# Kernel tuning notes

Hardware: AMD Instinct MI355X
Metric: run time of the kernel (lower is better)

Reference implementation:

```python
import jax, jax.numpy as jnp
import numpy as np

NPOINT, K = 1024, 16
BN_EPS = 1e-5


def farthest_point_sample(xyz, npoint):
    # xyz: [B, N, 3]. Deterministic start at index 0 (torch version uses randint).
    B, N, _ = xyz.shape

    def step(carry, _):
        distance, farthest = carry
        centroid = jnp.take_along_axis(xyz, farthest[:, None, None], axis=1)  # [B,1,3]
        dist = jnp.sum((xyz - centroid) ** 2, axis=-1)  # [B,N]
        distance = jnp.minimum(distance, dist)
        nxt = jnp.argmax(distance, axis=-1)
        return (distance, nxt), farthest

    init = (jnp.full((B, N), 1e10, dtype=xyz.dtype), jnp.zeros((B,), dtype=jnp.int32))
    _, cents = jax.lax.scan(step, init, None, length=npoint)
    return jnp.transpose(cents)  # [B, npoint]


def knn_idx(k, xyz, new_xyz):
    # squared distances [B,S,N] via ||a||^2 + ||b||^2 - 2 a.b (avoids [B,S,N,3] blowup)
    d = (jnp.sum(new_xyz ** 2, -1)[:, :, None]
         + jnp.sum(xyz ** 2, -1)[:, None, :]
         - 2.0 * jnp.einsum('bsc,bnc->bsn', new_xyz, xyz))
    _, idx = jax.lax.top_k(-d, k)  # k smallest distances
    return idx


def gather_points(points, idx):
    # points: [B,N,C], idx: [B,...] -> [B,...,C]
    return jax.vmap(lambda p, i: p[i])(points, idx)


def bn_train(x, gamma, beta):
    # BatchNorm1d in train mode: batch statistics, biased variance
    m = jnp.mean(x, axis=0)
    v = jnp.var(x, axis=0)
    return gamma * (x - m) * jax.lax.rsqrt(v + BN_EPS) + beta


def setup_inputs() -> dict:
    key = jax.random.key(0)
    ks = jax.random.split(key, 16)
    B, N, CIN, COUT = 8, 4096, 64, 128
    cin3 = CIN + 3          # 67
    ec = int(cin3 * 2.0)    # 134 (expand_ratio=2, hidden_ch arg is unused by InvResMLP)
    s = 0.05
    return {
        'xyz': jax.random.normal(ks[0], (B, N, 3), jnp.float32),
        'pts': jax.random.normal(ks[1], (B, N, CIN), jnp.float32),
        'fc1_w': jax.random.normal(ks[2], (cin3, ec), jnp.float32) * s,
        'fc1_b': jnp.zeros((ec,), jnp.float32),
        'bn1_g': jnp.ones((ec,), jnp.float32),
        'bn1_b': jnp.zeros((ec,), jnp.float32),
        'fc2_w': jax.random.normal(ks[3], (ec, ec), jnp.float32) * s,
        'fc2_b': jnp.zeros((ec,), jnp.float32),
        'bn2_g': jnp.ones((ec,), jnp.float32),
        'bn2_b': jnp.zeros((ec,), jnp.float32),
        'fc3_w': jax.random.normal(ks[4], (ec, COUT), jnp.float32) * s,
        'fc3_b': jnp.zeros((COUT,), jnp.float32),
        'bn3_g': jnp.ones((COUT,), jnp.float32),
        'bn3_b': jnp.zeros((COUT,), jnp.float32),
        'sc_w': jax.random.normal(ks[5], (cin3, COUT), jnp.float32) * s,
        'sc_b': jnp.zeros((COUT,), jnp.float32),
        'scbn_g': jnp.ones((COUT,), jnp.float32),
        'scbn_b': jnp.zeros((COUT,), jnp.float32),
    }


def reference(xyz, pts, fc1_w, fc1_b, bn1_g, bn1_b, fc2_w, fc2_b, bn2_g, bn2_b,
              fc3_w, fc3_b, bn3_g, bn3_b, sc_w, sc_b, scbn_g, scbn_b):
    # --- local_group: FPS + kNN grouping ---
    cent = farthest_point_sample(xyz, NPOINT)          # [B,S]
    new_xyz = gather_points(xyz, cent)                 # [B,S,3]
    idx = knn_idx(K, xyz, new_xyz)                     # [B,S,K]
    grouped_xyz = gather_points(xyz, idx)              # [B,S,K,3]
    grouped_pts = gather_points(pts, idx)              # [B,S,K,C]
    grouped_xyz_norm = grouped_xyz - new_xyz[:, :, None, :]
    x = jnp.concatenate([grouped_xyz_norm, grouped_pts], axis=-1)  # [B,S,K,C+3]

    # --- InvResMLP (pointwise, train-mode BN, dropout as identity) ---
    B, S, Kk, C = x.shape
    x = x.reshape(B * S * Kk, C)
    sc = bn_train(x @ sc_w + sc_b, scbn_g, scbn_b)
    h = jax.nn.relu(bn_train(x @ fc1_w + fc1_b, bn1_g, bn1_b))
    h = jax.nn.relu(bn_train(h @ fc2_w + fc2_b, bn2_g, bn2_b))
    h = bn_train(h @ fc3_w + fc3_b, bn3_g, bn3_b)
    h = jax.nn.relu(h + sc)
    feats = h.reshape(B, S, Kk, -1)

    new_pts = jnp.max(feats, axis=2)                   # [B,S,out_ch]
    return new_xyz, new_pts
```

## Files before the change

kernel.cpp:

```cpp
#include <hip/hip_runtime.h>
#include <cstdint>
#include <cstddef>

typedef short short8 __attribute__((ext_vector_type(8)));
typedef float f32x4 __attribute__((ext_vector_type(4)));
typedef unsigned long long u64x2 __attribute__((ext_vector_type(2)));

#define B_   8
#define N_   4096
#define S_   1024
#define K_   16
#define M_   131072
#define CIN_ 64

__device__ inline float bf2f(unsigned short u) {
    unsigned int v = ((unsigned int)u) << 16;
    return __builtin_bit_cast(float, v);
}
__device__ inline unsigned short f2bf(float f) {
    unsigned int u = __builtin_bit_cast(unsigned int, f);
    unsigned int lsb = (u >> 16) & 1u;
    u += 0x7fffu + lsb;
    return (unsigned short)(u >> 16);
}

template<int CTRL>
__device__ inline float dpp_maxf(float x) {
    int xi = __builtin_bit_cast(int, x);
    int yi = __builtin_amdgcn_update_dpp(0, xi, CTRL, 0xF, 0xF, true);
    return fmaxf(x, __builtin_bit_cast(float, yi));
}

__global__ __launch_bounds__(256) void fps_aux_kernel(
    const float* __restrict__ xyz, float* __restrict__ outxyz,
    const float* __restrict__ fc1_w, const float* __restrict__ sc_w,
    const float* __restrict__ fc2_w, const float* __restrict__ fc3_w,
    unsigned short* __restrict__ WT1, unsigned short* __restrict__ WT2,
    unsigned short* __restrict__ WT3, float* __restrict__ sqn)
{
    __shared__ float px_s[N_], py_s[N_], pz_s[N_];
    __shared__ float sOut[S_ * 3];
    __shared__ __attribute__((aligned(16))) unsigned long long sK[2][4];
    int t = threadIdx.x;

    if (blockIdx.x >= 8) {
        int aux = blockIdx.x - 8;
#pragma unroll
        for (int ch = 0; ch < 10; ch++) {
            int idx = (aux * 10 + ch) * 256 + t;
            if (idx < 13824) {
                int row = idx / 96, k = idx % 96;
                WT1[idx] = f2bf((k < 67 && row < 134) ? fc1_w[k * 134 + row] : 0.0f);
            } else if (idx < 26112) {
                int j = idx - 13824;
                int row = j / 96, k = j % 96;
                WT1[13824 + j] = f2bf((k < 67) ? sc_w[k * 128 + row] : 0.0f);
            } else if (idx < 49152) {
                int j = idx - 26112;
                int row = j / 160, k = j % 160;
                WT2[j] = f2bf((k < 134 && row < 134) ? fc2_w[k * 134 + row] : 0.0f);
            } else if (idx < 69632) {
                int j = idx - 49152;
                int row = j / 160, k = j % 160;
                WT3[j] = f2bf((k < 134) ? fc3_w[k * 128 + row] : 0.0f);
            } else {
                int i = idx - 69632;
                float x = xyz[i * 3 + 0], y = xyz[i * 3 + 1], z = xyz[i * 3 + 2];
                sqn[i] = __fadd_rn(__fadd_rn(__fmul_rn(x, x), __fmul_rn(y, y)),
                                   __fmul_rn(z, z));
            }
        }
        return;
    }

    int b = blockIdx.x;
    const float* xb = xyz + (size_t)b * N_ * 3;
    int w = t >> 6, l = t & 63;
    const int NP = 16;
    float px[NP], py[NP], pz[NP], dst[NP];
    {
        float flat[48];
        const float4* xb4 = (const float4*)xb + t * 12;
#pragma unroll
        for (int j = 0; j < 12; j++) {
            float4 v = xb4[j];
            flat[j * 4 + 0] = v.x; flat[j * 4 + 1] = v.y;
            flat[j * 4 + 2] = v.z; flat[j * 4 + 3] = v.w;
        }
#pragma unroll
        for (int i = 0; i < NP; i++) {
            int p = t * 16 + i;
            px[i] = flat[i * 3 + 0];
            py[i] = flat[i * 3 + 1];
            pz[i] = flat[i * 3 + 2];
            dst[i] = 1e10f;
            px_s[p] = px[i]; py_s[p] = py[i]; pz_s[p] = pz[i];
            asm volatile("" : "+v"(px[i]), "+v"(py[i]), "+v"(pz[i]));
        }
    }
    __syncthreads();
    float cx = px_s[0], cy = py_s[0], cz = pz_s[0];
    for (int s = 0; s < S_; s++) {
        if (t == 0) { sOut[s * 3 + 0] = cx; sOut[s * 3 + 1] = cy; sOut[s * 3 + 2] = cz; }
        if (s == S_ - 1) break;
        float bd = -1.0f; int bi = 0;
#pragma unroll
        for (int i = 0; i < NP; i++) {
            float dx = __fsub_rn(px[i], cx);
            float dy = __fsub_rn(py[i], cy);
            float dz = __fsub_rn(pz[i], cz);
            float d  = __fadd_rn(__fadd_rn(__fmul_rn(dx, dx), __fmul_rn(dy, dy)),
                                 __fmul_rn(dz, dz));
            float nd = fminf(dst[i], d);
            dst[i] = nd;
            if (nd > bd) bi = i;
            bd = fmaxf(bd, nd);
        }
        float m = bd;
        m = dpp_maxf<0xB1>(m);
        m = dpp_maxf<0x4E>(m);
        m = dpp_maxf<0x141>(m);
        m = dpp_maxf<0x140>(m);
        m = dpp_maxf<0x142>(m);
        m = dpp_maxf<0x143>(m);
        float bw = __builtin_bit_cast(float,
                       __builtin_amdgcn_readlane(__builtin_bit_cast(int, m), 63));
        unsigned long long msk = __ballot(bd == bw);
        int wl  = (int)__builtin_ctzll(msk);
        int wbi = __builtin_amdgcn_readlane(bi, wl);
        int pw  = (w * 64 + wl) * 16 + wbi;
        unsigned long long key =
            ((unsigned long long)__builtin_bit_cast(unsigned, bw) << 32) |
            (unsigned long long)(unsigned)(4095 - pw);
        int par = s & 1;
        if (l == 0) sK[par][w] = key;
        __syncthreads();
        u64x2 kA = *(u64x2*)&sK[par][0];
        u64x2 kB = *(u64x2*)&sK[par][2];
        unsigned long long ka = kA[0] > kA[1] ? kA[0] : kA[1];
        unsigned long long kb = kB[0] > kB[1] ? kB[0] : kB[1];
        unsigned long long g  = ka > kb ? ka : kb;
        int p = 4095 - (int)(g & 0xFFFu);
        cx = px_s[p]; cy = py_s[p]; cz = pz_s[p];
    }
    __syncthreads();
    float* ob = outxyz + (size_t)b * S_ * 3;
    for (int i = t; i < S_ * 3; i += 256) ob[i] = sOut[i];
}

__global__ __launch_bounds__(256) void knn_build(const float* __restrict__ xyz,
                                                 const float* __restrict__ sqn,
                                                 const float* __restrict__ newxyz,
                                                 const float* __restrict__ pts,
                                                 unsigned short* __restrict__ X)
{
    __shared__ int sNbr[4][16];
    int w = threadIdx.x >> 6, l = threadIdx.x & 63;
    int q = blockIdx.x * 4 + w;
    int b = q >> 10;
    const float* xb = xyz + (size_t)b * N_ * 3;
    const float* sb = sqn + (size_t)b * N_;
    float qx = newxyz[(size_t)q * 3 + 0];
    float qy = newxyz[(size_t)q * 3 + 1];
    float qz = newxyz[(size_t)q * 3 + 2];
    float sa = __fadd_rn(__fadd_rn(__fmul_rn(qx, qx), __fmul_rn(qy, qy)), __fmul_rn(qz, qz));

    float d16[16]; int i16[16];
#pragma unroll
    for (int j = 0; j < 16; j++) { d16[j] = 3.0e38f; i16[j] = -1; }
    for (int i = 0; i < N_ / 64; i++) {
        int n = i * 64 + l;
        float bx = xb[n * 3 + 0], by = xb[n * 3 + 1], bz = xb[n * 3 + 2];
        float dot = __fmaf_rn(qz, bz, __fmaf_rn(qy, by, __fmul_rn(qx, bx)));
        float d = __fsub_rn(__fadd_rn(sa, sb[n]), __fmul_rn(2.0f, dot));
        if (d < d16[0]) {
            d16[0] = d; i16[0] = n;
#pragma unroll
            for (int j = 0; j < 15; j++) {
                if (d16[j] < d16[j + 1]) {
                    float td = d16[j]; d16[j] = d16[j + 1]; d16[j + 1] = td;
                    int   ti = i16[j]; i16[j] = i16[j + 1]; i16[j + 1] = ti;
                }
            }
        }
    }
#pragma unroll
    for (int r = 0; r < 16; r++) {
        float cd = d16[15]; int cn = i16[15];
#pragma unroll
        for (int off = 1; off < 64; off <<= 1) {
            float od = __shfl_xor(cd, off);
            int   on = __shfl_xor(cn, off);
            if (od < cd || (od == cd && on < cn)) { cd = od; cn = on; }
        }
        if (l == 0) sNbr[w][r] = cn;
        if (i16[15] == cn) {
#pragma unroll
            for (int j = 15; j >= 1; j--) { d16[j] = d16[j - 1]; i16[j] = i16[j - 1]; }
            d16[0] = 3.0e38f; i16[0] = -1;
        }
    }
    __syncthreads();
    int row = l >> 2, seg = l & 3;
    int n = sNbr[w][row];
    const float* pr = pts + ((size_t)b * N_ + n) * CIN_;
    const float* xr = xyz + ((size_t)b * N_ + n) * 3;
    float v[24];
#pragma unroll
    for (int e = 0; e < 24; e++) {
        int c = seg * 24 + e;
        float val;
        if (c == 0)      val = xr[0] - qx;
        else if (c == 1) val = xr[1] - qy;
        else if (c == 2) val = xr[2] - qz;
        else if (c < 67) val = pr[c - 3];
        else             val = 0.0f;
        v[e] = val;
    }
    short8 s0, s1, s2;
#pragma unroll
    for (int e = 0; e < 8; e++) {
        s0[e] = (short)f2bf(v[e]);
        s1[e] = (short)f2bf(v[8 + e]);
        s2[e] = (short)f2bf(v[16 + e]);
    }
    unsigned short* xp = X + ((size_t)q * 16 + row) * 96 + seg * 24;
    *(short8*)xp = s0;
    *(short8*)(xp + 8) = s1;
    *(short8*)(xp + 16) = s2;
}

template<int KPAD, int NF, bool BNST>
__device__ __forceinline__ void gemm_core(
    const unsigned short* __restrict__ A, const unsigned short* __restrict__ Wt,
    unsigned short* __restrict__ Zo, float* __restrict__ sum, float* __restrict__ sq,
    int nreal, const float* __restrict__ ps, const float* __restrict__ pq,
    const float* __restrict__ pg, const float* __restrict__ pb,
    int r0, unsigned short* sBuf, float* sSt, float* sAC, int t)
{
    constexpr int AST = KPAD + 8;
    for (int i = t; i < NF * 32; i += 256) sSt[i] = 0.0f;
    if (BNST) {
        if (t < 160) {
            float a = 0.f, c = 0.f;
            if (t < 134) {
                const float inv = 1.0f / (float)M_;
                float m = ps[t] * inv;
                float var = pq[t] * inv - m * m;
                a = pg[t] * rsqrtf(var + 1e-5f);
                c = pb[t] - a * m;
            }
            sAC[2 * t] = a; sAC[2 * t + 1] = c;
        }
        __syncthreads();
#pragma unroll
        for (int c8 = 0; c8 < 10; c8++) {
            int chunk = c8 * 256 + t;
            int row = chunk / 20, col0 = (chunk % 20) * 8;
            short8 hv = {0, 0, 0, 0, 0, 0, 0, 0};
            if (col0 < 144) {
                short8 zv = *(const short8*)(A + (size_t)(r0 + row) * 144 + col0);
#pragma unroll
                for (int e = 0; e < 8; e++) {
                    float2 ac = *(float2*)&sAC[2 * (col0 + e)];
                    float v = fmaxf(ac.x * bf2f((unsigned short)zv[e]) + ac.y, 0.0f);
                    hv[e] = (short)f2bf(v);
                }
            }
            *(short8*)(sBuf + row * AST + col0) = hv;
        }
    } else {
#pragma unroll
        for (int c8 = 0; c8 < (128 * KPAD / 8) / 256; c8++) {
            int chunk = c8 * 256 + t;
            int row = chunk / (KPAD / 8), col0 = (chunk % (KPAD / 8)) * 8;
            *(short8*)(sBuf + row * AST + col0) =
                *(const short8*)(A + (size_t)(r0 + row) * KPAD + col0);
        }
    }
    __syncthreads();
    int w = t >> 6, l = t & 63, lhi = l >> 4, llo = l & 15;
    f32x4 acc[2][NF];
#pragma unroll
    for (int m = 0; m < 2; m++)
#pragma unroll
        for (int n = 0; n < NF; n++) acc[m][n] = (f32x4){0.f, 0.f, 0.f, 0.f};
#pragma unroll
    for (int ks = 0; ks < KPAD / 32; ks++) {
        short8 bfr[NF];
#pragma unroll
        for (int n = 0; n < NF; n++)
            bfr[n] = *(const short8*)(Wt + (size_t)(n * 16 + llo) * KPAD + ks * 32 + lhi * 8);
#pragma unroll
        for (int m = 0; m < 2; m++) {
            short8 afr = *(const short8*)(sBuf + (w * 32 + m * 16 + llo) * AST + ks * 32 + lhi * 8);
#pragma unroll
            for (int n = 0; n < NF; n++)
                acc[m][n] = __builtin_amdgcn_mfma_f32_16x16x32_bf16(afr, bfr[n], acc[m][n], 0, 0, 0);
        }
    }
    __syncthreads();
    constexpr int OST = NF * 16 + 8;
#pragma unroll
    for (int n = 0; n < NF; n++) {
        int c = n * 16 + llo;
        float ss = 0.f, sqv = 0.f;
#pragma unroll
        for (int m = 0; m < 2; m++) {
#pragma unroll
            for (int j = 0; j < 4; j++) {
                float v = acc[m][n][j];
                int row = w * 32 + m * 16 + lhi * 4 + j;
                sBuf[row * OST + c] = f2bf(v);
                ss += v; sqv += v * v;
            }
        }
        ss += __shfl_xor(ss, 16); ss += __shfl_xor(ss, 32);
        sqv += __shfl_xor(sqv, 16); sqv += __shfl_xor(sqv, 32);
        if (l < 16) { atomicAdd(&sSt[c * 2], ss); atomicAdd(&sSt[c * 2 + 1], sqv); }
    }
    __syncthreads();
#pragma unroll
    for (int c8 = 0; c8 < NF; c8++) {
        int chunk = c8 * 256 + t;
        int row = chunk / (NF * 2), cc = chunk % (NF * 2);
        *(short8*)(Zo + (size_t)(r0 + row) * (NF * 16) + cc * 8) =
            *(const short8*)(sBuf + row * OST + cc * 8);
    }
    for (int c = t; c < NF * 16; c += 256) {
        if (c < nreal) {
            atomicAdd(&sum[c], sSt[c * 2]);
            atomicAdd(&sq[c], sSt[c * 2 + 1]);
        }
    }
}

__global__ __launch_bounds__(256) void gemm1_fused(
    const unsigned short* __restrict__ X, const unsigned short* __restrict__ WT1,
    unsigned short* __restrict__ Z1, unsigned short* __restrict__ ZSC,
    float* s1, float* q1, float* ssc, float* qsc)
{
    __shared__ unsigned short sBuf[21504];
    __shared__ float sSt[288];
    int t = threadIdx.x;
    if (blockIdx.x < 1024)
        gemm_core<96, 9, false>(X, WT1, Z1, s1, q1, 134,
                                nullptr, nullptr, nullptr, nullptr,
                                blockIdx.x * 128, sBuf, sSt, nullptr, t);
    else
        gemm_core<96, 8, false>(X, WT1 + 13824, ZSC, ssc, qsc, 128,
                                nullptr, nullptr, nullptr, nullptr,
                                (blockIdx.x - 1024) * 128, sBuf, sSt, nullptr, t);
}

__global__ __launch_bounds__(256) void gemm_l2(
    const unsigned short* __restrict__ Zin, const unsigned short* __restrict__ WT,
    unsigned short* __restrict__ Zout, float* sum, float* sq,
    const float* ps, const float* pq, const float* pg, const float* pb)
{
    __shared__ unsigned short sBuf[21504];
    __shared__ float sSt[288];
    __shared__ float sAC[320];
    gemm_core<160, 9, true>(Zin, WT, Zout, sum, sq, 134, ps, pq, pg, pb,
                            blockIdx.x * 128, sBuf, sSt, sAC, threadIdx.x);
}

__global__ __launch_bounds__(256) void gemm_l3(
    const unsigned short* __restrict__ Zin, const unsigned short* __restrict__ WT,
    unsigned short* __restrict__ Zout, float* sum, float* sq,
    const float* ps, const float* pq, const float* pg, const float* pb)
{
    __shared__ unsigned short sBuf[21504];
    __shared__ float sSt[288];
    __shared__ float sAC[320];
    gemm_core<160, 8, true>(Zin, WT, Zout, sum, sq, 128, ps, pq, pg, pb,
                            blockIdx.x * 128, sBuf, sSt, sAC, threadIdx.x);
}

__global__ __launch_bounds__(256) void final_kernel(
    const unsigned short* __restrict__ Z3, const unsigned short* __restrict__ ZSC,
    const float* __restrict__ sum3, const float* __restrict__ sq3,
    const float* __restrict__ g3, const float* __restrict__ b3,
    const float* __restrict__ sumsc, const float* __restrict__ sqsc,
    const float* __restrict__ gsc, const float* __restrict__ bsc,
    float* __restrict__ out)
{
    __shared__ float sF[512];
    int t = threadIdx.x;
    if (t < 128) {
        const float inv = 1.0f / (float)M_;
        float m3 = sum3[t] * inv, v3 = sq3[t] * inv - m3 * m3;
        float a3 = g3[t] * rsqrtf(v3 + 1e-5f), c3 = b3[t] - a3 * m3;
        float ms = sumsc[t] * inv, vs = sqsc[t] * inv - ms * ms;
        float as = gsc[t] * rsqrtf(vs + 1e-5f), cs = bsc[t] - as * ms;
        sF[t * 4 + 0] = a3; sF[t * 4 + 1] = c3; sF[t * 4 + 2] = as; sF[t * 4 + 3] = cs;
    }
    __syncthreads();
    int tid = blockIdx.x * 256 + t;
    int bs = tid >> 4, ch0 = (tid & 15) * 8;
    float A3[8], C3[8], AS[8], CS[8], mx[8];
#pragma unroll
    for (int e = 0; e < 8; e++) {
        f32x4 f = *(f32x4*)&sF[(ch0 + e) * 4];
        A3[e] = f[0]; C3[e] = f[1]; AS[e] = f[2]; CS[e] = f[3];
        mx[e] = 0.0f;
    }
    const unsigned short* z3p = Z3 + (size_t)bs * 16 * 128 + ch0;
    const unsigned short* zsp = ZSC + (size_t)bs * 16 * 128 + ch0;
#pragma unroll
    for (int k = 0; k < 16; k++) {
        short8 z3 = *(const short8*)(z3p + (size_t)k * 128);
        short8 zs = *(const short8*)(zsp + (size_t)k * 128);
#pragma unroll
        for (int e = 0; e < 8; e++) {
            float y = fmaxf(A3[e] * bf2f((unsigned short)z3[e]) + C3[e]
                            + AS[e] * bf2f((unsigned short)zs[e]) + CS[e], 0.0f);
            mx[e] = fmaxf(mx[e], y);
        }
    }
    float* op = out + 24576 + (size_t)bs * 128 + ch0;
#pragma unroll
    for (int e = 0; e < 8; e++) op[e] = mx[e];
}

#define WS_STATS 0
#define WS_WT1   8192
#define WS_WT2   61440
#define WS_WT3   108544
#define WS_SQN   149760
#define WS_X     281088
#define WS_Z1    25447424
#define WS_ZSC   63196416
#define WS_Z2    96751104

extern "C" void kernel_launch(void* const* d_in, const int* in_sizes, int n_in,
                              void* d_out, int out_size, void* d_ws, size_t ws_size,
                              hipStream_t stream)
{
    const float* xyz    = (const float*)d_in[0];
    const float* pts    = (const float*)d_in[1];
    const float* fc1_w  = (const float*)d_in[2];
    const float* bn1_g  = (const float*)d_in[4];
    const float* bn1_b  = (const float*)d_in[5];
    const float* fc2_w  = (const float*)d_in[6];
    const float* bn2_g  = (const float*)d_in[8];
    const float* bn2_b  = (const float*)d_in[9];
    const float* fc3_w  = (const float*)d_in[10];
    const float* bn3_g  = (const float*)d_in[12];
    const float* bn3_b  = (const float*)d_in[13];
    const float* sc_w   = (const float*)d_in[14];
    const float* scbn_g = (const float*)d_in[16];
    const float* scbn_b = (const float*)d_in[17];

    char* ws = (char*)d_ws;
    float* st = (float*)(ws + WS_STATS);
    float* bn1_sum = st + 0,    *bn1_sq = st + 136;
    float* bnsc_sum = st + 272, *bnsc_sq = st + 400;
    float* bn2_sum = st + 528,  *bn2_sq = st + 664;
    float* bn3_sum = st + 800,  *bn3_sq = st + 928;

    unsigned short* WT1 = (unsigned short*)(ws + WS_WT1);
    unsigned short* WT2 = (unsigned short*)(ws + WS_WT2);
    unsigned short* WT3 = (unsigned short*)(ws + WS_WT3);
    float* SQN = (float*)(ws + WS_SQN);
    unsigned short* X   = (unsigned short*)(ws + WS_X);
    unsigned short* Z1  = (unsigned short*)(ws + WS_Z1);
    unsigned short* ZSC = (unsigned short*)(ws + WS_ZSC);
    unsigned short* Z2  = (unsigned short*)(ws + WS_Z2);
    unsigned short* Z3  = Z1;
    float* out = (float*)d_out;

    hipMemsetAsync(ws + WS_STATS, 0, 1056 * 4, stream);

    fps_aux_kernel<<<48, 256, 0, stream>>>(xyz, out, fc1_w, sc_w, fc2_w, fc3_w,
                                           WT1, WT2, WT3, SQN);
    knn_build<<<2048, 256, 0, stream>>>(xyz, SQN, out, pts, X);

    gemm1_fused<<<2048, 256, 0, stream>>>(X, WT1, Z1, ZSC,
                                          bn1_sum, bn1_sq, bnsc_sum, bnsc_sq);
    gemm_l2<<<1024, 256, 0, stream>>>(Z1, WT2, Z2, bn2_sum, bn2_sq,
                                      bn1_sum, bn1_sq, bn1_g, bn1_b);
    gemm_l3<<<1024, 256, 0, stream>>>(Z2, WT3, Z3, bn3_sum, bn3_sq,
                                      bn2_sum, bn2_sq, bn2_g, bn2_b);

    final_kernel<<<512, 256, 0, stream>>>(Z3, ZSC, bn3_sum, bn3_sq, bn3_g, bn3_b,
                                          bnsc_sum, bnsc_sq, scbn_g, scbn_b, out);
}
```

Before: 958.0 us.

## Fuse pipeline into cooperative persistent megakernel overlapping FPS with kNN

Replaces the six-kernel sequence with a single cooperative persistent kernel. Eight blocks run farthest-point sampling and publish progress watermarks every 64 centroids. Worker blocks spin on those watermarks so kNN grouping runs alongside FPS, and the GEMM and BN layers are separated by software grid barriers. The change targets the serial FPS latency and the launch gaps between stages. It adds spin-wait and grid-barrier overhead, limits the grid to 512 blocks, and keeps the old launch path as a fallback if the cooperative launch fails. It also swaps the bf16 packing to v_cvt_pk_bf16_f32.

```diff
diff --git a/kernel.cpp b/kernel.cpp
--- a/kernel.cpp
+++ b/kernel.cpp
@@ -23,12 +23,435 @@
     u += 0x7fffu + lsb;
     return (unsigned short)(u >> 16);
 }
+__device__ inline unsigned cvtpk_bf16(float lo, float hi) {
+    unsigned r; asm("v_cvt_pk_bf16_f32 %0, %1, %2" : "=v"(r) : "v"(lo), "v"(hi)); return r;
+}
+__device__ inline short8 pack8_bf16(const float* v) {
+    uint4 u;
+    u.x = cvtpk_bf16(v[0], v[1]); u.y = cvtpk_bf16(v[2], v[3]);
+    u.z = cvtpk_bf16(v[4], v[5]); u.w = cvtpk_bf16(v[6], v[7]);
+    return __builtin_bit_cast(short8, u);
+}
 
 template<int CTRL>
 __device__ inline float dpp_maxf(float x) {
     int xi = __builtin_bit_cast(int, x);
     int yi = __builtin_amdgcn_update_dpp(0, xi, CTRL, 0xF, 0xF, true);
     return fmaxf(x, __builtin_bit_cast(float, yi));
+}
+
+template<int KPAD, int NF, bool BNST>
+__device__ __forceinline__ void gemm_core(
+    const unsigned short* __restrict__ A, const unsigned short* __restrict__ Wt,
+    unsigned short* __restrict__ Zo, float* __restrict__ sum, float* __restrict__ sq,
+    int nreal, const float* __restrict__ ps, const float* __restrict__ pq,
+    const float* __restrict__ pg, const float* __restrict__ pb,
+    int r0, unsigned short* sBuf, float* sSt, float* sAC, int t)
+{
+    __syncthreads();
+    constexpr int AST = KPAD + 8;
+    for (int i = t; i < NF * 32; i += 256) sSt[i] = 0.0f;
+    if (BNST) {
+        if (t < 160) {
+            float a = 0.f, c = 0.f;
+            if (t < 134) {
+                const float inv = 1.0f / (float)M_;
+                float m = ps[t] * inv;
+                float var = pq[t] * inv - m * m;
+                a = pg[t] * rsqrtf(var + 1e-5f);
+                c = pb[t] - a * m;
+            }
+            sAC[2 * t] = a; sAC[2 * t + 1] = c;
+        }
+        __syncthreads();
+#pragma unroll
+        for (int c8 = 0; c8 < 10; c8++) {
+            int chunk = c8 * 256 + t;
+            int row = chunk / 20, col0 = (chunk % 20) * 8;
+            short8 hv = {0, 0, 0, 0, 0, 0, 0, 0};
+            if (col0 < 144) {
+                short8 zv = *(const short8*)(A + (size_t)(r0 + row) * 144 + col0);
+                float tmp[8];
+#pragma unroll
+                for (int e = 0; e < 8; e++) {
+                    float2 ac = *(float2*)&sAC[2 * (col0 + e)];
+                    tmp[e] = fmaxf(ac.x * bf2f((unsigned short)zv[e]) + ac.y, 0.0f);
+                }
+                hv = pack8_bf16(tmp);
+            }
+            *(short8*)(sBuf + row * AST + col0) = hv;
+        }
+    } else {
+#pragma unroll
+        for (int c8 = 0; c8 < (128 * KPAD / 8) / 256; c8++) {
+            int chunk = c8 * 256 + t;
+            int row = chunk / (KPAD / 8), col0 = (chunk % (KPAD / 8)) * 8;
+            *(short8*)(sBuf + row * AST + col0) =
+                *(const short8*)(A + (size_t)(r0 + row) * KPAD + col0);
+        }
+    }
+    __syncthreads();
+    int w = t >> 6, l = t & 63, lhi = l >> 4, llo = l & 15;
+    f32x4 acc[2][NF];
+#pragma unroll
+    for (int m = 0; m < 2; m++)
+#pragma unroll
+        for (int n = 0; n < NF; n++) acc[m][n] = (f32x4){0.f, 0.f, 0.f, 0.f};
+#pragma unroll
+    for (int ks = 0; ks < KPAD / 32; ks++) {
+        short8 bfr[NF];
+#pragma unroll
+        for (int n = 0; n < NF; n++)
+            bfr[n] = *(const short8*)(Wt + (size_t)(n * 16 + llo) * KPAD + ks * 32 + lhi * 8);
+#pragma unroll
+        for (int m = 0; m < 2; m++) {
+            short8 afr = *(const short8*)(sBuf + (w * 32 + m * 16 + llo) * AST + ks * 32 + lhi * 8);
+#pragma unroll
+            for (int n = 0; n < NF; n++)
+                acc[m][n] = __builtin_amdgcn_mfma_f32_16x16x32_bf16(afr, bfr[n], acc[m][n], 0, 0, 0);
+        }
+    }
+    __syncthreads();
+    constexpr int OST = NF * 16 + 8;
+#pragma unroll
+    for (int n = 0; n < NF; n++) {
+        int c = n * 16 + llo;
+        float ss = 0.f, sqv = 0.f;
+#pragma unroll
+        for (int m = 0; m < 2; m++) {
+#pragma unroll
+            for (int j = 0; j < 4; j++) {
+                float v = acc[m][n][j];
+                int row = w * 32 + m * 16 + lhi * 4 + j;
+                sBuf[row * OST + c] = f2bf(v);
+                ss += v; sqv += v * v;
+            }
+        }
+        ss += __shfl_xor(ss, 16); ss += __shfl_xor(ss, 32);
+        sqv += __shfl_xor(sqv, 16); sqv += __shfl_xor(sqv, 32);
+        if (l < 16) { atomicAdd(&sSt[c * 2], ss); atomicAdd(&sSt[c * 2 + 1], sqv); }
+    }
+    __syncthreads();
+#pragma unroll
+    for (int c8 = 0; c8 < NF; c8++) {
+        int chunk = c8 * 256 + t;
+        int row = chunk / (NF * 2), cc = chunk % (NF * 2);
+        *(short8*)(Zo + (size_t)(r0 + row) * (NF * 16) + cc * 8) =
+            *(const short8*)(sBuf + row * OST + cc * 8);
+    }
+    for (int c = t; c < NF * 16; c += 256) {
+        if (c < nreal) {
+            atomicAdd(&sum[c], sSt[c * 2]);
+            atomicAdd(&sq[c], sSt[c * 2 + 1]);
+        }
+    }
+}
+
+__device__ inline void gridbar(int* cnt, int* gen, int nblk, int t)
+{
+    __syncthreads();
+    __threadfence();
+    if (t == 0) {
+        int g = __hip_atomic_load(gen, __ATOMIC_RELAXED, __HIP_MEMORY_SCOPE_AGENT);
+        if (__hip_atomic_fetch_add(cnt, 1, __ATOMIC_ACQ_REL, __HIP_MEMORY_SCOPE_AGENT) == nblk - 1) {
+            __hip_atomic_store(cnt, 0, __ATOMIC_RELAXED, __HIP_MEMORY_SCOPE_AGENT);
+            __hip_atomic_store(gen, g + 1, __ATOMIC_RELEASE, __HIP_MEMORY_SCOPE_AGENT);
+        } else {
+            while (__hip_atomic_load(gen, __ATOMIC_ACQUIRE, __HIP_MEMORY_SCOPE_AGENT) == g)
+                __builtin_amdgcn_s_sleep(8);
+        }
+    }
+    __syncthreads();
+    __threadfence();
+}
+
+struct MegaArgs {
+    const float *xyz, *pts, *fc1_w, *sc_w, *fc2_w, *fc3_w;
+    const float *bn1_g, *bn1_b, *bn2_g, *bn2_b, *bn3_g, *bn3_b, *scbn_g, *scbn_b;
+    unsigned short *WT1, *WT2, *WT3;
+    float *SQN;
+    unsigned short *X, *Z1, *ZSC, *Z2;
+    float *st; int *wm; int *bar_cnt; int *bar_gen;
+    float *out;
+    int workers;
+};
+
+__global__ __launch_bounds__(256) void mega(MegaArgs A)
+{
+    __shared__ __attribute__((aligned(16))) char smem[61952];
+    int t = threadIdx.x;
+    int bid = blockIdx.x;
+    int nblk = gridDim.x;
+
+    float* st = A.st;
+    float* bn1_sum = st + 0,    *bn1_sq = st + 136;
+    float* bnsc_sum = st + 272, *bnsc_sq = st + 400;
+    float* bn2_sum = st + 528,  *bn2_sq = st + 664;
+    float* bn3_sum = st + 800,  *bn3_sq = st + 928;
+
+    if (bid < 8) {
+        float* px_s = (float*)smem;
+        float* py_s = px_s + 4096;
+        float* pz_s = px_s + 8192;
+        float* sOut = (float*)(smem + 49152);
+        unsigned long long* sK = (unsigned long long*)(smem + 61440);
+        int b = bid;
+        const float* xb = A.xyz + (size_t)b * N_ * 3;
+        float* ob = A.out + (size_t)b * S_ * 3;
+        int w = t >> 6, l = t & 63;
+        float px[16], py[16], pz[16], dst[16];
+        {
+            float flat[48];
+            const float4* xb4 = (const float4*)xb + t * 12;
+#pragma unroll
+            for (int j = 0; j < 12; j++) {
+                float4 v = xb4[j];
+                flat[j * 4 + 0] = v.x; flat[j * 4 + 1] = v.y;
+                flat[j * 4 + 2] = v.z; flat[j * 4 + 3] = v.w;
+            }
+#pragma unroll
+            for (int i = 0; i < 16; i++) {
+                int p = t * 16 + i;
+                px[i] = flat[i * 3 + 0];
+                py[i] = flat[i * 3 + 1];
+                pz[i] = flat[i * 3 + 2];
+                dst[i] = 1e10f;
+                px_s[p] = px[i]; py_s[p] = py[i]; pz_s[p] = pz[i];
+                asm volatile("" : "+v"(px[i]), "+v"(py[i]), "+v"(pz[i]));
+            }
+        }
+        __syncthreads();
+        float cx = px_s[0], cy = py_s[0], cz = pz_s[0];
+        for (int s = 0; s < S_; s++) {
+            if (t == 0) { sOut[s * 3 + 0] = cx; sOut[s * 3 + 1] = cy; sOut[s * 3 + 2] = cz; }
+            if ((s & 63) == 63 && w == 0) {
+                int base = (s - 63) * 3;
+                if (l < 48) {
+                    float4 v = *(float4*)&sOut[base + l * 4];
+                    *(float4*)&ob[base + l * 4] = v;
+                }
+                __threadfence();
+                if (t == 0)
+                    __hip_atomic_store(A.wm + b * 16, s + 1, __ATOMIC_RELEASE,
+                                       __HIP_MEMORY_SCOPE_AGENT);
+            }
+            if (s == S_ - 1) break;
+            float bd = -1.0f; int bi = 0;
+#pragma unroll
+            for (int i = 0; i < 16; i++) {
+                float dx = __fsub_rn(px[i], cx);
+                float dy = __fsub_rn(py[i], cy);
+                float dz = __fsub_rn(pz[i], cz);
+                float d  = __fadd_rn(__fadd_rn(__fmul_rn(dx, dx), __fmul_rn(dy, dy)),
+                                     __fmul_rn(dz, dz));
+                float nd = fminf(dst[i], d);
+                dst[i] = nd;
+                if (nd > bd) bi = i;
+                bd = fmaxf(bd, nd);
+            }
+            float m = bd;
+            m = dpp_maxf<0xB1>(m);
+            m = dpp_maxf<0x4E>(m);
+            m = dpp_maxf<0x141>(m);
+            m = dpp_maxf<0x140>(m);
+            m = dpp_maxf<0x142>(m);
+            m = dpp_maxf<0x143>(m);
+            float bw = __builtin_bit_cast(float,
+                           __builtin_amdgcn_readlane(__builtin_bit_cast(int, m), 63));
+            unsigned long long msk = __ballot(bd == bw);
+            int wl  = (int)__builtin_ctzll(msk);
+            int wbi = __builtin_amdgcn_readlane(bi, wl);
+            int pw  = (w * 64 + wl) * 16 + wbi;
+            unsigned long long key =
+                ((unsigned long long)__builtin_bit_cast(unsigned, bw) << 32) |
+                (unsigned long long)(unsigned)(4095 - pw);
+            int par = s & 1;
+            if (l == 0) sK[par * 4 + w] = key;
+            __syncthreads();
+            u64x2 kA = *(u64x2*)&sK[par * 4 + 0];
+            u64x2 kB = *(u64x2*)&sK[par * 4 + 2];
+            unsigned long long ka = kA[0] > kA[1] ? kA[0] : kA[1];
+            unsigned long long kb = kB[0] > kB[1] ? kB[0] : kB[1];
+            unsigned long long g  = ka > kb ? ka : kb;
+            int p = 4095 - (int)(g & 0xFFFu);
+            cx = px_s[p]; cy = py_s[p]; cz = pz_s[p];
+        }
+    } else {
+        int wk = bid - 8;
+        if (wk < 40) {
+#pragma unroll
+            for (int ch = 0; ch < 10; ch++) {
+                int idx = (wk * 10 + ch) * 256 + t;
+                if (idx < 13824) {
+                    int row = idx / 96, k = idx % 96;
+                    A.WT1[idx] = f2bf((k < 67 && row < 134) ? A.fc1_w[k * 134 + row] : 0.0f);
+                } else if (idx < 26112) {
+                    int j = idx - 13824;
+                    int row = j / 96, k = j % 96;
+                    A.WT1[13824 + j] = f2bf((k < 67) ? A.sc_w[k * 128 + row] : 0.0f);
+                } else if (idx < 49152) {
+                    int j = idx - 26112;
+                    int row = j / 160, k = j % 160;
+                    A.WT2[j] = f2bf((k < 134 && row < 134) ? A.fc2_w[k * 134 + row] : 0.0f);
+                } else if (idx < 69632) {
+                    int j = idx - 49152;
+                    int row = j / 160, k = j % 160;
+                    A.WT3[j] = f2bf((k < 134) ? A.fc3_w[k * 128 + row] : 0.0f);
+                }
+            }
+        }
+        float* sqnL = (float*)smem;
+        int* sNbr = (int*)(smem + 16384);
+        int b = wk & 7;
+        const float* xb = A.xyz + (size_t)b * N_ * 3;
+#pragma unroll
+        for (int i = 0; i < 16; i++) {
+            int p = i * 256 + t;
+            float x = xb[p * 3 + 0], y = xb[p * 3 + 1], z = xb[p * 3 + 2];
+            sqnL[p] = __fadd_rn(__fadd_rn(__fmul_rn(x, x), __fmul_rn(y, y)),
+                                __fmul_rn(z, z));
+        }
+        __syncthreads();
+        int w = t >> 6, l = t & 63;
+        for (int G = wk; G < 2048; G += A.workers) {
+            int sidx = (G >> 3) * 4 + w;
+            int q = b * 1024 + sidx;
+            while (__hip_atomic_load(A.wm + b * 16, __ATOMIC_ACQUIRE,
+                                     __HIP_MEMORY_SCOPE_AGENT) <= sidx)
+                __builtin_amdgcn_s_sleep(32);
+            float qx = A.out[(size_t)q * 3 + 0];
+            float qy = A.out[(size_t)q * 3 + 1];
+            float qz = A.out[(size_t)q * 3 + 2];
+            float sa = __fadd_rn(__fadd_rn(__fmul_rn(qx, qx), __fmul_rn(qy, qy)),
+                                 __fmul_rn(qz, qz));
+            float d16[16]; int i16[16];
+#pragma unroll
+            for (int j = 0; j < 16; j++) { d16[j] = 3.0e38f; i16[j] = -1; }
+            for (int i = 0; i < N_ / 64; i++) {
+                int n = i * 64 + l;
+                float bx = xb[n * 3 + 0], by = xb[n * 3 + 1], bz = xb[n * 3 + 2];
+                float dot = __fmaf_rn(qz, bz, __fmaf_rn(qy, by, __fmul_rn(qx, bx)));
+                float d = __fsub_rn(__fadd_rn(sa, sqnL[n]), __fmul_rn(2.0f, dot));
+                if (d < d16[0]) {
+                    d16[0] = d; i16[0] = n;
+#pragma unroll
+                    for (int j = 0; j < 15; j++) {
+                        if (d16[j] < d16[j + 1]) {
+                            float td = d16[j]; d16[j] = d16[j + 1]; d16[j + 1] = td;
+                            int   ti = i16[j]; i16[j] = i16[j + 1]; i16[j + 1] = ti;
+                        }
+                    }
+                }
+            }
+#pragma unroll
+            for (int r = 0; r < 16; r++) {
+                float cd = d16[15]; int cn = i16[15];
+#pragma unroll
+                for (int off = 1; off < 64; off <<= 1) {
+                    float od = __shfl_xor(cd, off);
+                    int   on = __shfl_xor(cn, off);
+                    if (od < cd || (od == cd && on < cn)) { cd = od; cn = on; }
+                }
+                if (l == 0) sNbr[w * 16 + r] = cn;
+                if (i16[15] == cn) {
+#pragma unroll
+                    for (int j = 15; j >= 1; j--) { d16[j] = d16[j - 1]; i16[j] = i16[j - 1]; }
+                    d16[0] = 3.0e38f; i16[0] = -1;
+                }
+            }
+            __syncthreads();
+            int row = l >> 2, seg = l & 3;
+            int n = sNbr[w * 16 + row];
+            const float* pr = A.pts + ((size_t)b * N_ + n) * CIN_;
+            const float* xr = A.xyz + ((size_t)b * N_ + n) * 3;
+            float v[24];
+#pragma unroll
+            for (int e = 0; e < 24; e++) {
+                int c = seg * 24 + e;
+                float val;
+                if (c == 0)      val = xr[0] - qx;
+                else if (c == 1) val = xr[1] - qy;
+                else if (c == 2) val = xr[2] - qz;
+                else if (c < 67) val = pr[c - 3];
+                else             val = 0.0f;
+                v[e] = val;
+            }
+            short8 s0 = pack8_bf16(v), s1 = pack8_bf16(v + 8), s2 = pack8_bf16(v + 16);
+            unsigned short* xp = A.X + ((size_t)q * 16 + row) * 96 + seg * 24;
+            *(short8*)xp = s0;
+            *(short8*)(xp + 8) = s1;
+            *(short8*)(xp + 16) = s2;
+            __syncthreads();
+        }
+    }
+    gridbar(A.bar_cnt, A.bar_gen, nblk, t);
+
+    {
+        unsigned short* sBuf = (unsigned short*)smem;
+        float* sSt = (float*)(smem + 43008);
+        float* sAC = (float*)(smem + 44160);
+        for (int tile = bid; tile < 2048; tile += nblk) {
+            if (tile < 1024)
+                gemm_core<96, 9, false>(A.X, A.WT1, A.Z1, bn1_sum, bn1_sq, 134,
+                                        nullptr, nullptr, nullptr, nullptr,
+                                        tile * 128, sBuf, sSt, sAC, t);
+            else
+                gemm_core<96, 8, false>(A.X, A.WT1 + 13824, A.ZSC, bnsc_sum, bnsc_sq, 128,
+                                        nullptr, nullptr, nullptr, nullptr,
+                                        (tile - 1024) * 128, sBuf, sSt, sAC, t);
+        }
+        gridbar(A.bar_cnt, A.bar_gen, nblk, t);
+        for (int tile = bid; tile < 1024; tile += nblk)
+            gemm_core<160, 9, true>(A.Z1, A.WT2, A.Z2, bn2_sum, bn2_sq, 134,
+                                    bn1_sum, bn1_sq, A.bn1_g, A.bn1_b,
+                                    tile * 128, sBuf, sSt, sAC, t);
+        gridbar(A.bar_cnt, A.bar_gen, nblk, t);
+        for (int tile = bid; tile < 1024; tile += nblk)
+            gemm_core<160, 8, true>(A.Z2, A.WT3, A.Z1 , bn3_sum, bn3_sq, 128,
+                                    bn2_sum, bn2_sq, A.bn2_g, A.bn2_b,
+                                    tile * 128, sBuf, sSt, sAC, t);
+        gridbar(A.bar_cnt, A.bar_gen, nblk, t);
+    }
+
+    {
+        float* sF = (float*)smem;
+        if (t < 128) {
+            const float inv = 1.0f / (float)M_;
+            float m3 = bn3_sum[t] * inv, v3 = bn3_sq[t] * inv - m3 * m3;
+            float a3 = A.bn3_g[t] * rsqrtf(v3 + 1e-5f), c3 = A.bn3_b[t] - a3 * m3;
+            float ms = bnsc_sum[t] * inv, vs = bnsc_sq[t] * inv - ms * ms;
+            float as = A.scbn_g[t] * rsqrtf(vs + 1e-5f), cs = A.scbn_b[t] - as * ms;
+            sF[t * 4 + 0] = a3; sF[t * 4 + 1] = c3; sF[t * 4 + 2] = as; sF[t * 4 + 3] = cs;
+        }
+        __syncthreads();
+        for (int c = bid; c < 512; c += nblk) {
+            int tid = c * 256 + t;
+            int bs = tid >> 4, ch0 = (tid & 15) * 8;
+            float A3[8], C3[8], AS[8], CS[8], mx[8];
+#pragma unroll
+            for (int e = 0; e < 8; e++) {
+                f32x4 f = *(f32x4*)&sF[(ch0 + e) * 4];
+                A3[e] = f[0]; C3[e] = f[1]; AS[e] = f[2]; CS[e] = f[3];
+                mx[e] = 0.0f;
+            }
+            const unsigned short* z3p = A.Z1 + (size_t)bs * 16 * 128 + ch0;
+            const unsigned short* zsp = A.ZSC + (size_t)bs * 16 * 128 + ch0;
+#pragma unroll
+            for (int k = 0; k < 16; k++) {
+                short8 z3 = *(const short8*)(z3p + (size_t)k * 128);
+                short8 zs = *(const short8*)(zsp + (size_t)k * 128);
+#pragma unroll
+                for (int e = 0; e < 8; e++) {
+                    float y = fmaxf(A3[e] * bf2f((unsigned short)z3[e]) + C3[e]
+                                    + AS[e] * bf2f((unsigned short)zs[e]) + CS[e], 0.0f);
+                    mx[e] = fmaxf(mx[e], y);
+                }
+            }
+            float* op = A.out + 24576 + (size_t)bs * 128 + ch0;
+#pragma unroll
+            for (int e = 0; e < 8; e++) op[e] = mx[e];
+        }
+    }
 }
 
 __global__ __launch_bounds__(256) void fps_aux_kernel(
@@ -42,7 +465,6 @@
     __shared__ float sOut[S_ * 3];
     __shared__ __attribute__((aligned(16))) unsigned long long sK[2][4];
     int t = threadIdx.x;
-
     if (blockIdx.x >= 8) {
         int aux = blockIdx.x - 8;
 #pragma unroll
@@ -72,12 +494,10 @@
         }
         return;
     }
-
     int b = blockIdx.x;
     const float* xb = xyz + (size_t)b * N_ * 3;
     int w = t >> 6, l = t & 63;
-    const int NP = 16;
-    float px[NP], py[NP], pz[NP], dst[NP];
+    float px[16], py[16], pz[16], dst[16];
     {
         float flat[48];
         const float4* xb4 = (const float4*)xb + t * 12;
@@ -88,11 +508,9 @@
             flat[j * 4 + 2] = v.z; flat[j * 4 + 3] = v.w;
         }
 #pragma unroll
-        for (int i = 0; i < NP; i++) {
+        for (int i = 0; i < 16; i++) {
             int p = t * 16 + i;
-            px[i] = flat[i * 3 + 0];
-            py[i] = flat[i * 3 + 1];
-            pz[i] = flat[i * 3 + 2];
+            px[i] = flat[i * 3 + 0]; py[i] = flat[i * 3 + 1]; pz[i] = flat[i * 3 + 2];
             dst[i] = 1e10f;
             px_s[p] = px[i]; py_s[p] = py[i]; pz_s[p] = pz[i];
             asm volatile("" : "+v"(px[i]), "+v"(py[i]), "+v"(pz[i]));
@@ -105,7 +523,7 @@
         if (s == S_ - 1) break;
         float bd = -1.0f; int bi = 0;
 #pragma unroll
-        for (int i = 0; i < NP; i++) {
+        for (int i = 0; i < 16; i++) {
             float dx = __fsub_rn(px[i], cx);
             float dy = __fsub_rn(py[i], cy);
             float dz = __fsub_rn(pz[i], cz);
@@ -117,12 +535,8 @@
             bd = fmaxf(bd, nd);
         }
         float m = bd;
-        m = dpp_maxf<0xB1>(m);
-        m = dpp_maxf<0x4E>(m);
-        m = dpp_maxf<0x141>(m);
-        m = dpp_maxf<0x140>(m);
-        m = dpp_maxf<0x142>(m);
-        m = dpp_maxf<0x143>(m);
+        m = dpp_maxf<0xB1>(m); m = dpp_maxf<0x4E>(m); m = dpp_maxf<0x141>(m);
+        m = dpp_maxf<0x140>(m); m = dpp_maxf<0x142>(m); m = dpp_maxf<0x143>(m);
         float bw = __builtin_bit_cast(float,
                        __builtin_amdgcn_readlane(__builtin_bit_cast(int, m), 63));
         unsigned long long msk = __ballot(bd == bw);
@@ -164,7 +578,6 @@
     float qy = newxyz[(size_t)q * 3 + 1];
     float qz = newxyz[(size_t)q * 3 + 2];
     float sa = __fadd_rn(__fadd_rn(__fmul_rn(qx, qx), __fmul_rn(qy, qy)), __fmul_rn(qz, qz));
-
     float d16[16]; int i16[16];
 #pragma unroll
     for (int j = 0; j < 16; j++) { d16[j] = 3.0e38f; i16[j] = -1; }
@@ -217,124 +630,13 @@
         else             val = 0.0f;
         v[e] = val;
     }
-    short8 s0, s1, s2;
-#pragma unroll
-    for (int e = 0; e < 8; e++) {
-        s0[e] = (short)f2bf(v[e]);
-        s1[e] = (short)f2bf(v[8 + e]);
-        s2[e] = (short)f2bf(v[16 + e]);
-    }
+    short8 s0 = pack8_bf16(v), s1 = pack8_bf16(v + 8), s2 = pack8_bf16(v + 16);
     unsigned short* xp = X + ((size_t)q * 16 + row) * 96 + seg * 24;
     *(short8*)xp = s0;
     *(short8*)(xp + 8) = s1;
     *(short8*)(xp + 16) = s2;
 }
 
-template<int KPAD, int NF, bool BNST>
-__device__ __forceinline__ void gemm_core(
-    const unsigned short* __restrict__ A, const unsigned short* __restrict__ Wt,
-    unsigned short* __restrict__ Zo, float* __restrict__ sum, float* __restrict__ sq,
-    int nreal, const float* __restrict__ ps, const float* __restrict__ pq,
-    const float* __restrict__ pg, const float* __restrict__ pb,
-    int r0, unsigned short* sBuf, float* sSt, float* sAC, int t)
-{
-    constexpr int AST = KPAD + 8;
-    for (int i = t; i < NF * 32; i += 256) sSt[i] = 0.0f;
-    if (BNST) {
-        if (t < 160) {
-            float a = 0.f, c = 0.f;
-            if (t < 134) {
-                const float inv = 1.0f / (float)M_;
-                float m = ps[t] * inv;
-                float var = pq[t] * inv - m * m;
-                a = pg[t] * rsqrtf(var + 1e-5f);
-                c = pb[t] - a * m;
-            }
-            sAC[2 * t] = a; sAC[2 * t + 1] = c;
-        }
-        __syncthreads();
-#pragma unroll
-        for (int c8 = 0; c8 < 10; c8++) {
-            int chunk = c8 * 256 + t;
-            int row = chunk / 20, col0 = (chunk % 20) * 8;
-            short8 hv = {0, 0, 0, 0, 0, 0, 0, 0};
-            if (col0 < 144) {
-                short8 zv = *(const short8*)(A + (size_t)(r0 + row) * 144 + col0);
-#pragma unroll
-                for (int e = 0; e < 8; e++) {
-                    float2 ac = *(float2*)&sAC[2 * (col0 + e)];
-                    float v = fmaxf(ac.x * bf2f((unsigned short)zv[e]) + ac.y, 0.0f);
-                    hv[e] = (short)f2bf(v);
-                }
-            }
-            *(short8*)(sBuf + row * AST + col0) = hv;
-        }
-    } else {
-#pragma unroll
-        for (int c8 = 0; c8 < (128 * KPAD / 8) / 256; c8++) {
-            int chunk = c8 * 256 + t;
-            int row = chunk / (KPAD / 8), col0 = (chunk % (KPAD / 8)) * 8;
-            *(short8*)(sBuf + row * AST + col0) =
-                *(const short8*)(A + (size_t)(r0 + row) * KPAD + col0);
-        }
-    }
-    __syncthreads();
-    int w = t >> 6, l = t & 63, lhi = l >> 4, llo = l & 15;
-    f32x4 acc[2][NF];
-#pragma unroll
-    for (int m = 0; m < 2; m++)
-#pragma unroll
-        for (int n = 0; n < NF; n++) acc[m][n] = (f32x4){0.f, 0.f, 0.f, 0.f};
-#pragma unroll
-    for (int ks = 0; ks < KPAD / 32; ks++) {
-        short8 bfr[NF];
-#pragma unroll
-        for (int n = 0; n < NF; n++)
-            bfr[n] = *(const short8*)(Wt + (size_t)(n * 16 + llo) * KPAD + ks * 32 + lhi * 8);
-#pragma unroll
-        for (int m = 0; m < 2; m++) {
-            short8 afr = *(const short8*)(sBuf + (w * 32 + m * 16 + llo) * AST + ks * 32 + lhi * 8);
-#pragma unroll
-            for (int n = 0; n < NF; n++)
-                acc[m][n] = __builtin_amdgcn_mfma_f32_16x16x32_bf16(afr, bfr[n], acc[m][n], 0, 0, 0);
-        }
-    }
-    __syncthreads();
-    constexpr int OST = NF * 16 + 8;
-#pragma unroll
-    for (int n = 0; n < NF; n++) {
-        int c = n * 16 + llo;
-        float ss = 0.f, sqv = 0.f;
-#pragma unroll
-        for (int m = 0; m < 2; m++) {
-#pragma unroll
-            for (int j = 0; j < 4; j++) {
-                float v = acc[m][n][j];
-                int row = w * 32 + m * 16 + lhi * 4 + j;
-                sBuf[row * OST + c] = f2bf(v);
-                ss += v; sqv += v * v;
-            }
-        }
-        ss += __shfl_xor(ss, 16); ss += __shfl_xor(ss, 32);
-        sqv += __shfl_xor(sqv, 16); sqv += __shfl_xor(sqv, 32);
-        if (l < 16) { atomicAdd(&sSt[c * 2], ss); atomicAdd(&sSt[c * 2 + 1], sqv); }
-    }
-    __syncthreads();
-#pragma unroll
-    for (int c8 = 0; c8 < NF; c8++) {
-        int chunk = c8 * 256 + t;
-        int row = chunk / (NF * 2), cc = chunk % (NF * 2);
-        *(short8*)(Zo + (size_t)(r0 + row) * (NF * 16) + cc * 8) =
-            *(const short8*)(sBuf + row * OST + cc * 8);
-    }
-    for (int c = t; c < NF * 16; c += 256) {
-        if (c < nreal) {
-            atomicAdd(&sum[c], sSt[c * 2]);
-            atomicAdd(&sq[c], sSt[c * 2 + 1]);
-        }
-    }
-}
-
 __global__ __launch_bounds__(256) void gemm1_fused(
     const unsigned short* __restrict__ X, const unsigned short* __restrict__ WT1,
     unsigned short* __restrict__ Z1, unsigned short* __restrict__ ZSC,
@@ -342,15 +644,16 @@
 {
     __shared__ unsigned short sBuf[21504];
     __shared__ float sSt[288];
+    __shared__ float sAC[320];
     int t = threadIdx.x;
     if (blockIdx.x < 1024)
         gemm_core<96, 9, false>(X, WT1, Z1, s1, q1, 134,
                                 nullptr, nullptr, nullptr, nullptr,
-                                blockIdx.x * 128, sBuf, sSt, nullptr, t);
+                                blockIdx.x * 128, sBuf, sSt, sAC, t);
     else
         gemm_core<96, 8, false>(X, WT1 + 13824, ZSC, ssc, qsc, 128,
                                 nullptr, nullptr, nullptr, nullptr,
-                                (blockIdx.x - 1024) * 128, sBuf, sSt, nullptr, t);
+                                (blockIdx.x - 1024) * 128, sBuf, sSt, sAC, t);
 }
 
 __global__ __launch_bounds__(256) void gemm_l2(
@@ -424,6 +727,9 @@
 }
 
 #define WS_STATS 0
+#define WS_WM    4224
+#define WS_BCNT  4736
+#define WS_BGEN  4800
 #define WS_WT1   8192
 #define WS_WT2   61440
 #define WS_WT3   108544
@@ -467,22 +773,44 @@
     unsigned short* Z1  = (unsigned short*)(ws + WS_Z1);
     unsigned short* ZSC = (unsigned short*)(ws + WS_ZSC);
     unsigned short* Z2  = (unsigned short*)(ws + WS_Z2);
-    unsigned short* Z3  = Z1;
     float* out = (float*)d_out;
 
-    hipMemsetAsync(ws + WS_STATS, 0, 1056 * 4, stream);
-
-    fps_aux_kernel<<<48, 256, 0, stream>>>(xyz, out, fc1_w, sc_w, fc2_w, fc3_w,
-                                           WT1, WT2, WT3, SQN);
-    knn_build<<<2048, 256, 0, stream>>>(xyz, SQN, out, pts, X);
-
-    gemm1_fused<<<2048, 256, 0, stream>>>(X, WT1, Z1, ZSC,
-                                          bn1_sum, bn1_sq, bnsc_sum, bnsc_sq);
-    gemm_l2<<<1024, 256, 0, stream>>>(Z1, WT2, Z2, bn2_sum, bn2_sq,
-                                      bn1_sum, bn1_sq, bn1_g, bn1_b);
-    gemm_l3<<<1024, 256, 0, stream>>>(Z2, WT3, Z3, bn3_sum, bn3_sq,
-                                      bn2_sum, bn2_sq, bn2_g, bn2_b);
-
-    final_kernel<<<512, 256, 0, stream>>>(Z3, ZSC, bn3_sum, bn3_sq, bn3_g, bn3_b,
-                                          bnsc_sum, bnsc_sq, scbn_g, scbn_b, out);
-}
+    hipMemsetAsync(ws, 0, 4864, stream);
+
+    int occ = 0;
+    bool launched = false;
+    if (hipOccupancyMaxActiveBlocksPerMultiprocessor(&occ, mega, 256, 0) == hipSuccess
+        && occ > 0) {
+        int blocks = occ * 256;
+        if (blocks > 512) blocks = 512;
+        int workers = ((blocks - 8) / 8) * 8;
+        if (workers >= 40) {
+            MegaArgs ma;
+            ma.xyz = xyz; ma.pts = pts; ma.fc1_w = fc1_w; ma.sc_w = sc_w;
+            ma.fc2_w = fc2_w; ma.fc3_w = fc3_w;
+            ma.bn1_g = bn1_g; ma.bn1_b = bn1_b; ma.bn2_g = bn2_g; ma.bn2_b = bn2_b;
+            ma.bn3_g = bn3_g; ma.bn3_b = bn3_b; ma.scbn_g = scbn_g; ma.scbn_b = scbn_b;
+            ma.WT1 = WT1; ma.WT2 = WT2; ma.WT3 = WT3; ma.SQN = SQN;
+            ma.X = X; ma.Z1 = Z1; ma.ZSC = ZSC; ma.Z2 = Z2;
+            ma.st = st; ma.wm = (int*)(ws + WS_WM);
+            ma.bar_cnt = (int*)(ws + WS_BCNT); ma.bar_gen = (int*)(ws + WS_BGEN);
+            ma.out = out; ma.workers = workers;
+            void* kargs[] = { &ma };
+            launched = (hipLaunchCooperativeKernel((const void*)mega,
+                            dim3(workers + 8), dim3(256), kargs, 0, stream) == hipSuccess);
+        }
+    }
+    if (!launched) {
+        fps_aux_kernel<<<48, 256, 0, stream>>>(xyz, out, fc1_w, sc_w, fc2_w, fc3_w,
+                                               WT1, WT2, WT3, SQN);
+        knn_build<<<2048, 256, 0, stream>>>(xyz, SQN, out, pts, X);
+        gemm1_fused<<<2048, 256, 0, stream>>>(X, WT1, Z1, ZSC,
+                                              bn1_sum, bn1_sq, bnsc_sum, bnsc_sq);
+        gemm_l2<<<1024, 256, 0, stream>>>(Z1, WT2, Z2, bn2_sum, bn2_sq,
+                                          bn1_sum, bn1_sq, bn1_g, bn1_b);
+        gemm_l3<<<1024, 256, 0, stream>>>(Z2, WT3, Z1, bn3_sum, bn3_sq,
+                                          bn2_sum, bn2_sq, bn2_g, bn2_b);
+        final_kernel<<<512, 256, 0, stream>>>(Z1, ZSC, bn3_sum, bn3_sq, bn3_g, bn3_b,
+                                              bnsc_sum, bnsc_sq, scbn_g, scbn_b, out);
+    }
+}
```

Measured after the change: 959.7 us. No clear change (+0.2%).
